# Kernel tuning notes

Measured on AMD Instinct MI355X. Metric: run time of the kernel, lower is better.

The kernel has to match this reference:

```python
import jax, jax.numpy as jnp
import numpy as np

E = 768      # embed_size
H = 12       # heads
L = 4        # num_length (stacked blocks)
N = 3072     # sequence length (and max_length)
FF = 4 * E   # feed-forward hidden
EPS = 1e-5


def layer_norm(x, g, b):
    mu = jnp.mean(x, axis=-1, keepdims=True)
    var = jnp.mean((x - mu) ** 2, axis=-1, keepdims=True)
    return (x - mu) / jnp.sqrt(var + EPS) * g + b


def setup_inputs() -> dict:
    key = jax.random.key(0)
    ks = jax.random.split(key, 12)
    inp = {
        "x": jax.random.normal(ks[0], (1, N, 768), dtype=jnp.float32),
        "mask": jnp.ones((1, N), dtype=jnp.int32),
        # 0.05 scale so word_encoding outputs have |.|>1 and survive the .long() truncation
        "W_word": jax.random.normal(ks[1], (E, 768), dtype=jnp.float32) * 0.05,
        "b_word": jnp.zeros((E,), dtype=jnp.float32),
        "pos_emb": jax.random.normal(ks[2], (N, E), dtype=jnp.float32),
        "Wq": jax.random.normal(ks[3], (L, E, E), dtype=jnp.float32) * 0.02,
        "Wk": jax.random.normal(ks[4], (L, E, E), dtype=jnp.float32) * 0.02,
        "Wv": jax.random.normal(ks[5], (L, E, E), dtype=jnp.float32) * 0.02,
        "Wo": jax.random.normal(ks[6], (L, E, E), dtype=jnp.float32) * 0.02,
        "W1": jax.random.normal(ks[7], (L, FF, E), dtype=jnp.float32) * 0.02,
        "b1": jnp.zeros((L, FF), dtype=jnp.float32),
        "W2": jax.random.normal(ks[8], (L, E, FF), dtype=jnp.float32) * 0.02,
        "b2": jnp.zeros((L, E), dtype=jnp.float32),
        "g1": jnp.ones((L, E), dtype=jnp.float32),
        "beta1": jnp.zeros((L, E), dtype=jnp.float32),
        "g2": jnp.ones((L, E), dtype=jnp.float32),
        "beta2": jnp.zeros((L, E), dtype=jnp.float32),
    }
    return inp


def reference(x, mask, W_word, b_word, pos_emb, Wq, Wk, Wv, Wo,
              W1, b1, W2, b2, g1, beta1, g2, beta2):
    # mask is squeezed then passed, but the original uses a non-inplace
    # masked_fill whose result is discarded -> mask has NO effect on the math.
    xs = x[0]                                # [N, 768]
    h = xs @ W_word.T + b_word               # word_encoding -> [N, E]
    h = jnp.trunc(h)                         # faithful to `x = x.long()` (cast truncation)
    n = h.shape[0]
    out = (h + pos_emb[:n])[None]            # [1, N, E]; dropout is identity (eval)
    d = E // H
    scale = jnp.asarray(E ** 0.5, out.dtype)  # softmax scaled by sqrt(embed_size)
    for l in range(L):
        q = (out @ Wq[l].T).reshape(1, n, H, d)
        k = (out @ Wk[l].T).reshape(1, n, H, d)
        v = (out @ Wv[l].T).reshape(1, n, H, d)
        energy = jnp.einsum('nqhd,nkhd->nhqk', q, k)      # [1, H, N, N]
        attn = jax.nn.softmax(energy / scale, axis=3)
        a = jnp.einsum('nhqk,nkhd->nqhd', attn, v).reshape(1, n, E) @ Wo[l].T
        xm = layer_norm(a + out, g1[l], beta1[l])
        y = jax.nn.relu(xm @ W1[l].T + b1[l]) @ W2[l].T + b2[l]
        out = layer_norm(xm + y, g2[l], beta2[l])
    return jnp.mean(out, axis=1, keepdims=True)          # [1, 1, E]
```

## Files before the change

kernel.cpp:

```cpp
#include <hip/hip_runtime.h>

#define E_  768
#define N_  3072
#define L_  4
#define H_  12
#define FF_ 3072
#define LDQKV 2304
#define SCL_ 0.052058744f

typedef short bf16x8 __attribute__((ext_vector_type(8)));
typedef short s16x4  __attribute__((ext_vector_type(4)));
typedef float f32x4  __attribute__((ext_vector_type(4)));
typedef __fp16 h16x2 __attribute__((ext_vector_type(2)));
typedef _Float16 f16x4 __attribute__((ext_vector_type(4)));
typedef _Float16 f16x8 __attribute__((ext_vector_type(8)));

__device__ __forceinline__ short f2bf(float f) {
  union { float f; unsigned u; } v; v.f = f;
  unsigned r = v.u + 0x7fffu + ((v.u >> 16) & 1u);
  return (short)(r >> 16);
}
__device__ __forceinline__ float bf2f(short s) {
  union { unsigned u; float f; } v; v.u = ((unsigned)(unsigned short)s) << 16;
  return v.f;
}

__device__ __forceinline__ void gld_lds16(const void* g, void* l) {
  __builtin_amdgcn_global_load_lds(
      (const __attribute__((address_space(1))) unsigned int*)g,
      (__attribute__((address_space(3))) unsigned int*)l, 16, 0, 0);
}

__global__ __launch_bounds__(256) void gemm_bt_kernel(
    const short* __restrict__ A, const short* __restrict__ B,
    const float* __restrict__ bias, float* __restrict__ Cf,
    short* __restrict__ Cb, _Float16* __restrict__ Vt,
    int Nd, int lda, int ldb, int kcnt, size_t czstride, int relu)
{
  alignas(16) __shared__ short As[128 * 32];
  alignas(16) __shared__ short Bs[128 * 32];
  const int tid = threadIdx.x;
  const int w = tid >> 6, lane = tid & 63;
  const int quad = lane >> 4, cl = lane & 15;
  const int wr = w >> 1, wc = w & 1;
  const int row0 = blockIdx.y * 128, col0 = blockIdx.x * 128;
  const int koff = blockIdx.z * kcnt;
  A += koff; B += koff;
  if (Cf) Cf += (size_t)blockIdx.z * czstride;
  const int srow = lane >> 2;
  const int scol = (((lane & 3) ^ ((lane >> 3) & 3)) * 8);
  const int rsw = (quad ^ ((cl >> 1) & 3)) * 8;
  const f32x4 fz = {0.f, 0.f, 0.f, 0.f};
  f32x4 acc[4][4];
#pragma unroll
  for (int i = 0; i < 4; i++)
#pragma unroll
    for (int j = 0; j < 4; j++) acc[i][j] = fz;

  const int nk = kcnt >> 5;
  for (int kt = 0; kt < nk; kt++) {
    const int k0 = kt << 5;
#pragma unroll
    for (int i = 0; i < 2; i++) {
      const int chunk = w * 2 + i;
      gld_lds16(A + (size_t)(row0 + chunk * 16 + srow) * lda + k0 + scol, As + chunk * 512);
      gld_lds16(B + (size_t)(col0 + chunk * 16 + srow) * ldb + k0 + scol, Bs + chunk * 512);
    }
    __syncthreads();
    bf16x8 af[4], bfr[4];
#pragma unroll
    for (int mt = 0; mt < 4; mt++)
      af[mt] = *(const bf16x8*)(As + (wr * 64 + mt * 16 + cl) * 32 + rsw);
#pragma unroll
    for (int nt = 0; nt < 4; nt++)
      bfr[nt] = *(const bf16x8*)(Bs + (wc * 64 + nt * 16 + cl) * 32 + rsw);
#pragma unroll
    for (int mt = 0; mt < 4; mt++)
#pragma unroll
      for (int nt = 0; nt < 4; nt++)
        acc[mt][nt] = __builtin_amdgcn_mfma_f32_16x16x32_bf16(af[mt], bfr[nt], acc[mt][nt], 0, 0, 0);
    __syncthreads();
  }
#pragma unroll
  for (int mt = 0; mt < 4; mt++)
#pragma unroll
    for (int nt = 0; nt < 4; nt++) {
      const int col = col0 + wc * 64 + nt * 16 + cl;
      const float bv = bias ? bias[col] : 0.f;
#pragma unroll
      for (int r = 0; r < 4; r++) {
        const int row = row0 + wr * 64 + mt * 16 + quad * 4 + r;
        float v2 = acc[mt][nt][r] + bv;
        if (relu) v2 = fmaxf(v2, 0.f);
        if (Cf) Cf[(size_t)row * Nd + col] = v2;
        if (Cb) Cb[(size_t)row * Nd + col] = f2bf(v2);
      }
      if (Vt && col >= 1536) {
        const int d = col - 1536;
        const int rowb = row0 + wr * 64 + mt * 16 + quad * 4;
        f16x4 vo;
#pragma unroll
        for (int r = 0; r < 4; r++) vo[r] = (_Float16)acc[mt][nt][r];
        *(f16x4*)(Vt + (size_t)d * N_ + rowb) = vo;
      }
    }
}

__global__ __launch_bounds__(256) void flash_kernel(
    const short* __restrict__ QKV, const _Float16* __restrict__ Vt,
    float* __restrict__ Op, float* __restrict__ Ml)
{
  alignas(16) __shared__ short Ks[64 * 64];
  alignas(16) __shared__ _Float16 Vs[64 * 64];
  const int tid = threadIdx.x;
  const int w = tid >> 6, lane = tid & 63;
  const int quad = lane >> 4, cl = lane & 15;
  const int q0 = blockIdx.x * 64, h = blockIdx.y, s = blockIdx.z;
  const int hoff = h * 64;
  const f32x4 fz = {0.f, 0.f, 0.f, 0.f};
  const int qrow = q0 + w * 16 + cl;
  const short* qp = QKV + (size_t)qrow * LDQKV + hoff;
  const bf16x8 bq0 = *(const bf16x8*)(qp + quad * 8);
  const bf16x8 bq1 = *(const bf16x8*)(qp + 32 + quad * 8);

  const int strow = lane >> 3;
  const int stcol = ((lane & 7) ^ strow) * 8;
  const short* kp0 = QKV + (size_t)(s * 768 + w * 16 + strow) * LDQKV + 768 + hoff + stcol;
  const short* kp1 = kp0 + 8 * LDQKV;
  const _Float16* vp0 = Vt + (size_t)(hoff + w * 16 + strow) * N_ + s * 768 + stcol;
  const _Float16* vp1 = vp0 + 8 * N_;
  short* ksd = Ks + w * 1024;
  _Float16* vsd = Vs + w * 1024;

  const int swz = cl & 7;
  const short* kf0 = Ks + cl * 64 + ((quad ^ swz) * 8);
  const short* kf1 = Ks + cl * 64 + (((quad + 4) ^ swz) * 8);
  const _Float16* vf0 = Vs + cl * 64 + (((0 + (quad >> 1)) ^ swz) * 8) + (quad & 1) * 4;
  const _Float16* vf1 = Vs + cl * 64 + (((2 + (quad >> 1)) ^ swz) * 8) + (quad & 1) * 4;
  const _Float16* vf2 = Vs + cl * 64 + (((4 + (quad >> 1)) ^ swz) * 8) + (quad & 1) * 4;
  const _Float16* vf3 = Vs + cl * 64 + (((6 + (quad >> 1)) ^ swz) * 8) + (quad & 1) * 4;

  f32x4 Oa[4];
#pragma unroll
  for (int t = 0; t < 4; t++) Oa[t] = fz;
  float l = 0.f;

  for (int kb = 0; kb < 12; kb++) {
    gld_lds16(kp0, ksd);
    gld_lds16(kp1, ksd + 512);
    gld_lds16(vp0, vsd);
    gld_lds16(vp1, vsd + 512);
    kp0 += 64 * LDQKV; kp1 += 64 * LDQKV; vp0 += 64; vp1 += 64;
    __syncthreads();
    f32x4 S[4];
#pragma unroll
    for (int t = 0; t < 4; t++) {
      const bf16x8 ak0 = *(const bf16x8*)(kf0 + t * 1024);
      const bf16x8 ak1 = *(const bf16x8*)(kf1 + t * 1024);
      f32x4 z = fz;
      z = __builtin_amdgcn_mfma_f32_16x16x32_bf16(ak0, bq0, z, 0, 0, 0);
      S[t] = __builtin_amdgcn_mfma_f32_16x16x32_bf16(ak1, bq1, z, 0, 0, 0);
    }
    f16x4 pf[4];
#pragma unroll
    for (int t = 0; t < 4; t++) {
      const float p0 = __builtin_amdgcn_exp2f(S[t][0]);
      const float p1 = __builtin_amdgcn_exp2f(S[t][1]);
      const float p2 = __builtin_amdgcn_exp2f(S[t][2]);
      const float p3 = __builtin_amdgcn_exp2f(S[t][3]);
      l += (p0 + p1) + (p2 + p3);
      const h16x2 lo = __builtin_amdgcn_cvt_pkrtz(p0, p1);
      const h16x2 hi = __builtin_amdgcn_cvt_pkrtz(p2, p3);
      pf[t][0] = (_Float16)lo[0]; pf[t][1] = (_Float16)lo[1];
      pf[t][2] = (_Float16)hi[0]; pf[t][3] = (_Float16)hi[1];
    }
#pragma unroll
    for (int td = 0; td < 4; td++) {
      Oa[td] = __builtin_amdgcn_mfma_f32_16x16x16f16(*(const f16x4*)(vf0 + td * 1024), pf[0], Oa[td], 0, 0, 0);
      Oa[td] = __builtin_amdgcn_mfma_f32_16x16x16f16(*(const f16x4*)(vf1 + td * 1024), pf[1], Oa[td], 0, 0, 0);
      Oa[td] = __builtin_amdgcn_mfma_f32_16x16x16f16(*(const f16x4*)(vf2 + td * 1024), pf[2], Oa[td], 0, 0, 0);
      Oa[td] = __builtin_amdgcn_mfma_f32_16x16x16f16(*(const f16x4*)(vf3 + td * 1024), pf[3], Oa[td], 0, 0, 0);
    }
    __syncthreads();
  }
  l += __shfl_xor(l, 16);
  l += __shfl_xor(l, 32);
  float* op = Op + ((size_t)s * N_ + qrow) * E_ + hoff;
#pragma unroll
  for (int td = 0; td < 4; td++)
#pragma unroll
    for (int r = 0; r < 4; r++)
      op[td * 16 + quad * 4 + r] = Oa[td][r];
  if (quad == 0)
    Ml[((size_t)s * H_ + h) * N_ + qrow] = l;
}

__global__ __launch_bounds__(256) void merge_kernel(
    const float* __restrict__ Op, const float* __restrict__ Ml,
    short* __restrict__ atb)
{
  const int idx = blockIdx.x * 256 + threadIdx.x;
  const int n = idx / 192, c4 = idx % 192;
  const int e0 = c4 * 4, h = e0 >> 6;
  float den = 0.f;
  f32x4 num = {0.f, 0.f, 0.f, 0.f};
#pragma unroll
  for (int s = 0; s < 4; s++) {
    den += Ml[((size_t)s * H_ + h) * N_ + n];
    const f32x4 o = *(const f32x4*)(Op + ((size_t)s * N_ + n) * E_ + e0);
#pragma unroll
    for (int j = 0; j < 4; j++) num[j] += o[j];
  }
  const float inv = 1.f / den;
  s16x4 ob;
#pragma unroll
  for (int j = 0; j < 4; j++) ob[j] = f2bf(num[j] * inv);
  *(s16x4*)(atb + (size_t)n * E_ + e0) = ob;
}

__global__ __launch_bounds__(256) void wordenc_fin_kernel(
    const float* __restrict__ p0, const float* __restrict__ p1,
    const float* __restrict__ bw, const float* __restrict__ pos,
    float* __restrict__ of, short* __restrict__ ob)
{
  const int idx = blockIdx.x * 256 + threadIdx.x;
  const size_t e4 = (size_t)idx * 4;
  const int cc = (int)(e4 % E_);
  const f32x4 a = *(const f32x4*)(p0 + e4);
  const f32x4 b = *(const f32x4*)(p1 + e4);
  const f32x4 bwv = *(const f32x4*)(bw + cc);
  const f32x4 pv = *(const f32x4*)(pos + e4);
  f32x4 o; s16x4 obv;
#pragma unroll
  for (int j = 0; j < 4; j++) {
    o[j] = truncf(a[j] + b[j] + bwv[j]) + pv[j];
    obv[j] = f2bf(o[j]);
  }
  *(f32x4*)(of + e4) = o;
  *(s16x4*)(ob + e4) = obv;
}

__global__ __launch_bounds__(256) void resid_ln_kernel(
    const float* __restrict__ a0, const float* __restrict__ a1,
    const float* __restrict__ a2, const float* __restrict__ a3,
    const float* __restrict__ b,
    const float* __restrict__ g, const float* __restrict__ bet,
    const float* __restrict__ bias,
    float* __restrict__ of, short* __restrict__ ob)
{
  const int row = blockIdx.x, tid = threadIdx.x;
  const int w = tid >> 6, lane = tid & 63;
  __shared__ float red[8];
  const size_t base = (size_t)row * E_;
  float v[3]; float s = 0.f;
#pragma unroll
  for (int j = 0; j < 3; j++) {
    const int cc = tid + j * 256;
    float t = (a0[base + cc] + a1[base + cc]) + (a2[base + cc] + a3[base + cc]) + b[base + cc];
    if (bias) t += bias[cc];
    v[j] = t;
    s += t;
  }
#pragma unroll
  for (int msk = 1; msk < 64; msk <<= 1) s += __shfl_xor(s, msk);
  if (lane == 0) red[w] = s;
  __syncthreads();
  const float mean = (red[0] + red[1] + red[2] + red[3]) * (1.f / E_);
  float s2 = 0.f;
#pragma unroll
  for (int j = 0; j < 3; j++) { const float d = v[j] - mean; s2 += d * d; }
#pragma unroll
  for (int msk = 1; msk < 64; msk <<= 1) s2 += __shfl_xor(s2, msk);
  if (lane == 0) red[4 + w] = s2;
  __syncthreads();
  const float var = (red[4] + red[5] + red[6] + red[7]) * (1.f / E_);
  const float rstd = rsqrtf(var + 1e-5f);
#pragma unroll
  for (int j = 0; j < 3; j++) {
    const int cc = tid + j * 256;
    const float o = (v[j] - mean) * rstd * g[cc] + bet[cc];
    of[base + cc] = o;
    ob[base + cc] = f2bf(o);
  }
}

__global__ __launch_bounds__(256) void prep_kernel(
    const float* __restrict__ Wq, const float* __restrict__ Wk,
    const float* __restrict__ Wv, const float* __restrict__ Wo,
    const float* __restrict__ W1, const float* __restrict__ W2,
    const float* __restrict__ Ww, const float* __restrict__ x,
    short* __restrict__ wqkv, short* __restrict__ wo_b,
    short* __restrict__ w1_b, short* __restrict__ w2_b,
    short* __restrict__ whl, short* __restrict__ xhl)
{
  int g = blockIdx.x * 256 + threadIdx.x;
  const int EEg = 589824;
  const int FEg = 2359296;
  if (g < 3 * EEg) {
    const int which = g / EEg;
    const int gi = g - which * EEg;
    const float* src = which == 0 ? Wq : (which == 1 ? Wk : Wv);
    const float scale = which == 0 ? SCL_ : 1.f;
    const size_t e4 = (size_t)gi * 4;
    const int lidx = (int)(e4 / (E_ * E_));
    const size_t rem = e4 % (E_ * E_);
    const f32x4 v = *(const f32x4*)(src + e4);
    s16x4 o;
#pragma unroll
    for (int q = 0; q < 4; q++) o[q] = f2bf(v[q] * scale);
    *(s16x4*)(wqkv + ((size_t)lidx * 3 + which) * E_ * E_ + rem) = o;
    return;
  }
  g -= 3 * EEg;
  if (g < EEg) {
    const size_t e4 = (size_t)g * 4;
    const f32x4 v = *(const f32x4*)(Wo + e4);
    s16x4 o;
#pragma unroll
    for (int q = 0; q < 4; q++) o[q] = f2bf(v[q]);
    *(s16x4*)(wo_b + e4) = o;
    return;
  }
  g -= EEg;
  if (g < FEg) {
    const size_t e4 = (size_t)g * 4;
    const f32x4 v = *(const f32x4*)(W1 + e4);
    s16x4 o;
#pragma unroll
    for (int q = 0; q < 4; q++) o[q] = f2bf(v[q]);
    *(s16x4*)(w1_b + e4) = o;
    return;
  }
  g -= FEg;
  if (g < FEg) {
    const size_t e4 = (size_t)g * 4;
    const f32x4 v = *(const f32x4*)(W2 + e4);
    s16x4 o;
#pragma unroll
    for (int q = 0; q < 4; q++) o[q] = f2bf(v[q]);
    *(s16x4*)(w2_b + e4) = o;
    return;
  }
  g -= FEg;
  if (g < 147456) {
    const size_t e4 = (size_t)g * 4;
    const int c = (int)(e4 / E_);
    const int k = (int)(e4 % E_);
    const f32x4 v = *(const f32x4*)(Ww + e4);
    s16x4 hi, lo;
#pragma unroll
    for (int q = 0; q < 4; q++) {
      hi[q] = f2bf(v[q]);
      lo[q] = f2bf(v[q] - bf2f(hi[q]));
    }
    short* base = whl + (size_t)c * LDQKV + k;
    *(s16x4*)(base) = hi;
    *(s16x4*)(base + 768) = hi;
    *(s16x4*)(base + 1536) = lo;
    return;
  }
  g -= 147456;
  {
    const size_t e4 = (size_t)g * 4;
    const int n = (int)(e4 / E_);
    const int k = (int)(e4 % E_);
    const f32x4 v = *(const f32x4*)(x + e4);
    s16x4 hi, lo;
#pragma unroll
    for (int q = 0; q < 4; q++) {
      hi[q] = f2bf(v[q]);
      lo[q] = f2bf(v[q] - bf2f(hi[q]));
    }
    short* base = xhl + (size_t)n * LDQKV + k;
    *(s16x4*)(base) = hi;
    *(s16x4*)(base + 768) = lo;
    *(s16x4*)(base + 1536) = hi;
  }
}

__global__ void colmean_kernel(const float* __restrict__ src, float* __restrict__ out)
{
  const int c = blockIdx.x * 256 + threadIdx.x;
  const int r0 = blockIdx.y * 128;
  float s = 0.f;
  for (int r = 0; r < 128; r++) s += src[(size_t)(r0 + r) * E_ + c];
  atomicAdd(&out[c], s * (1.f / N_));
}

extern "C" void kernel_launch(void* const* d_in, const int* in_sizes, int n_in,
                              void* d_out, int out_size, void* d_ws, size_t ws_size,
                              hipStream_t stream)
{
  (void)in_sizes; (void)n_in; (void)out_size; (void)ws_size;
  const float* x     = (const float*)d_in[0];
  const float* Wword = (const float*)d_in[2];
  const float* bword = (const float*)d_in[3];
  const float* pos   = (const float*)d_in[4];
  const float* Wq    = (const float*)d_in[5];
  const float* Wk    = (const float*)d_in[6];
  const float* Wv    = (const float*)d_in[7];
  const float* Wo    = (const float*)d_in[8];
  const float* W1    = (const float*)d_in[9];
  const float* b1    = (const float*)d_in[10];
  const float* W2    = (const float*)d_in[11];
  const float* b2    = (const float*)d_in[12];
  const float* g1    = (const float*)d_in[13];
  const float* be1   = (const float*)d_in[14];
  const float* g2    = (const float*)d_in[15];
  const float* be2   = (const float*)d_in[16];

  char* p = (char*)d_ws;
  auto take = [&](size_t bytes) { char* q = p; p += (bytes + 255) & ~(size_t)255; return q; };
  const size_t EE = (size_t)E_ * E_;
  const size_t NE = (size_t)N_ * E_;
  const size_t FE = (size_t)FF_ * E_;

  short* wqkv_b = (short*)take(L_ * 3 * EE * 2);
  short* wo_b   = (short*)take(L_ * EE * 2);
  short* w1_b   = (short*)take(L_ * FE * 2);
  short* w2_b   = (short*)take(L_ * FE * 2);
  short* whl    = (short*)take((size_t)E_ * LDQKV * 2);
  float* outf   = (float*)take(NE * 4);
  short* outb   = (short*)take(NE * 2);
  float* xmf    = (float*)take(NE * 4);
  short* xmb    = (short*)take(NE * 2);
  short* qkvb   = (short*)take((size_t)N_ * LDQKV * 2);
  float* Op     = (float*)take(4 * NE * 4);
  float* part4  = (float*)take(4 * NE * 4);
  float* Ml     = (float*)take((size_t)4 * H_ * N_ * 4);

  short* xhl  = qkvb;
  short* y1b  = (short*)Op;
  _Float16* vtb = (_Float16*)xmf;
  short* atb  = outb;

  prep_kernel<<<dim3(30528), dim3(256), 0, stream>>>(
      Wq, Wk, Wv, Wo, W1, W2, Wword, x,
      wqkv_b, wo_b, w1_b, w2_b, whl, xhl);

  gemm_bt_kernel<<<dim3(6, 24, 2), dim3(256), 0, stream>>>(
      xhl, whl, nullptr, Op, nullptr, nullptr, E_, LDQKV, LDQKV, 1152, NE, 0);
  wordenc_fin_kernel<<<dim3(2304), dim3(256), 0, stream>>>(
      Op, Op + NE, bword, pos, outf, outb);

  for (int l = 0; l < L_; l++) {
    gemm_bt_kernel<<<dim3(18, 24, 1), dim3(256), 0, stream>>>(
        outb, wqkv_b + l * 3 * EE, nullptr, nullptr, qkvb, vtb, LDQKV, E_, E_, E_, 0, 0);
    flash_kernel<<<dim3(48, 12, 4), dim3(256), 0, stream>>>(qkvb, vtb, Op, Ml);
    merge_kernel<<<dim3(2304), dim3(256), 0, stream>>>(Op, Ml, atb);
    gemm_bt_kernel<<<dim3(6, 24, 4), dim3(256), 0, stream>>>(
        atb, wo_b + l * EE, nullptr, Op, nullptr, nullptr, E_, E_, E_, 192, NE, 0);
    resid_ln_kernel<<<dim3(N_), dim3(256), 0, stream>>>(
        Op, Op + NE, Op + 2 * NE, Op + 3 * NE, outf,
        g1 + l * E_, be1 + l * E_, nullptr, xmf, xmb);
    gemm_bt_kernel<<<dim3(24, 24, 1), dim3(256), 0, stream>>>(
        xmb, w1_b + l * FE, b1 + l * FF_, nullptr, y1b, nullptr, FF_, E_, E_, E_, 0, 1);
    gemm_bt_kernel<<<dim3(6, 24, 4), dim3(256), 0, stream>>>(
        y1b, w2_b + l * FE, nullptr, part4, nullptr, nullptr, E_, FF_, FF_, 768, NE, 0);
    resid_ln_kernel<<<dim3(N_), dim3(256), 0, stream>>>(
        part4, part4 + NE, part4 + 2 * NE, part4 + 3 * NE, xmf,
        g2 + l * E_, be2 + l * E_, b2 + l * E_, outf, outb);
  }
  hipMemsetAsync(d_out, 0, E_ * sizeof(float), stream);
  colmean_kernel<<<dim3(3, 24), dim3(256), 0, stream>>>(outf, (float*)d_out);
}
```

Baseline: 994.8 us.

## Restructure flash attention: per-wave key split, double-buffered LDS, in-block reduction

The flash kernel now gives each wave all 64 query rows of the block and its own slice of the keys, instead of a 16-row slice sharing keys with the other waves. Each wave streams its keys through a private double-buffered LDS area using async global-to-LDS loads and vmcnt waits, so the per-iteration block barriers go away. The four waves' partial outputs are then reduced through LDS at the end. This halves the key split across blocks, so the merge kernel reads two partials instead of four. It costs more accumulator registers (16 f32x4 per wave) and a final LDS reduction, which may lower occupancy. Separately, the prep kernel processes two elements per thread with half as many blocks.

```diff
diff --git a/kernel.cpp b/kernel.cpp
--- a/kernel.cpp
+++ b/kernel.cpp
@@ -13,7 +13,6 @@
 typedef float f32x4  __attribute__((ext_vector_type(4)));
 typedef __fp16 h16x2 __attribute__((ext_vector_type(2)));
 typedef _Float16 f16x4 __attribute__((ext_vector_type(4)));
-typedef _Float16 f16x8 __attribute__((ext_vector_type(8)));
 
 __device__ __forceinline__ short f2bf(float f) {
   union { float f; unsigned u; } v; v.f = f;
@@ -110,89 +109,157 @@
     const short* __restrict__ QKV, const _Float16* __restrict__ Vt,
     float* __restrict__ Op, float* __restrict__ Ml)
 {
-  alignas(16) __shared__ short Ks[64 * 64];
-  alignas(16) __shared__ _Float16 Vs[64 * 64];
+  alignas(16) __shared__ short KV[16640];
   const int tid = threadIdx.x;
   const int w = tid >> 6, lane = tid & 63;
   const int quad = lane >> 4, cl = lane & 15;
   const int q0 = blockIdx.x * 64, h = blockIdx.y, s = blockIdx.z;
   const int hoff = h * 64;
   const f32x4 fz = {0.f, 0.f, 0.f, 0.f};
-  const int qrow = q0 + w * 16 + cl;
-  const short* qp = QKV + (size_t)qrow * LDQKV + hoff;
-  const bf16x8 bq0 = *(const bf16x8*)(qp + quad * 8);
-  const bf16x8 bq1 = *(const bf16x8*)(qp + 32 + quad * 8);
-
-  const int strow = lane >> 3;
-  const int stcol = ((lane & 7) ^ strow) * 8;
-  const short* kp0 = QKV + (size_t)(s * 768 + w * 16 + strow) * LDQKV + 768 + hoff + stcol;
+
+  bf16x8 bq[4][2];
+#pragma unroll
+  for (int qt = 0; qt < 4; qt++)
+#pragma unroll
+    for (int c = 0; c < 2; c++)
+      bq[qt][c] = *(const bf16x8*)(QKV + (size_t)(q0 + qt * 16 + cl) * LDQKV + hoff + c * 32 + quad * 8);
+
+  const int kr0 = s * 1536 + w * 384;
+  const short* kp0 = QKV + (size_t)(kr0 + (lane >> 3)) * LDQKV + 768 + hoff + ((lane & 7) ^ (lane >> 3)) * 8;
   const short* kp1 = kp0 + 8 * LDQKV;
-  const _Float16* vp0 = Vt + (size_t)(hoff + w * 16 + strow) * N_ + s * 768 + stcol;
-  const _Float16* vp1 = vp0 + 8 * N_;
-  short* ksd = Ks + w * 1024;
-  _Float16* vsd = Vs + w * 1024;
-
-  const int swz = cl & 7;
-  const short* kf0 = Ks + cl * 64 + ((quad ^ swz) * 8);
-  const short* kf1 = Ks + cl * 64 + (((quad + 4) ^ swz) * 8);
-  const _Float16* vf0 = Vs + cl * 64 + (((0 + (quad >> 1)) ^ swz) * 8) + (quad & 1) * 4;
-  const _Float16* vf1 = Vs + cl * 64 + (((2 + (quad >> 1)) ^ swz) * 8) + (quad & 1) * 4;
-  const _Float16* vf2 = Vs + cl * 64 + (((4 + (quad >> 1)) ^ swz) * 8) + (quad & 1) * 4;
-  const _Float16* vf3 = Vs + cl * 64 + (((6 + (quad >> 1)) ^ swz) * 8) + (quad & 1) * 4;
-
-  f32x4 Oa[4];
-#pragma unroll
-  for (int t = 0; t < 4; t++) Oa[t] = fz;
-  float l = 0.f;
-
-  for (int kb = 0; kb < 12; kb++) {
-    gld_lds16(kp0, ksd);
-    gld_lds16(kp1, ksd + 512);
-    gld_lds16(vp0, vsd);
-    gld_lds16(vp1, vsd + 512);
-    kp0 += 64 * LDQKV; kp1 += 64 * LDQKV; vp0 += 64; vp1 += 64;
-    __syncthreads();
+  const _Float16* vp0 = Vt + (size_t)(hoff + (lane >> 1)) * N_ + kr0 + (lane & 1) * 8;
+  const _Float16* vp1 = vp0 + 32 * N_;
+  short* kb0 = KV + w * 4096;
+  short* kb1 = KV + w * 4096 + 1024;
+  short* vb0 = KV + w * 4096 + 2048;
+  short* vb1 = KV + w * 4096 + 3072;
+
+  f32x4 Oa[16];
+#pragma unroll
+  for (int t = 0; t < 16; t++) Oa[t] = fz;
+  float l4[4] = {0.f, 0.f, 0.f, 0.f};
+
+  gld_lds16(kp0, kb0); gld_lds16(kp1, kb0 + 512);
+  gld_lds16(vp0, vb0); gld_lds16(vp1, vb0 + 512);
+  kp0 += 16 * LDQKV; kp1 += 16 * LDQKV; vp0 += 16; vp1 += 16;
+
+  for (int it = 0; it < 24; it++) {
+    const int cur = it & 1;
+    {
+      short* kn = cur ? kb0 : kb1;
+      short* vn = cur ? vb0 : vb1;
+      gld_lds16(kp0, kn); gld_lds16(kp1, kn + 512);
+      gld_lds16(vp0, vn); gld_lds16(vp1, vn + 512);
+      kp0 += 16 * LDQKV; kp1 += 16 * LDQKV; vp0 += 16; vp1 += 16;
+    }
+    asm volatile("s_waitcnt vmcnt(4)" ::: "memory");
+    const short* kc = (cur ? kb1 : kb0) + cl * 64;
+    const _Float16* vc = (const _Float16*)(cur ? vb1 : vb0);
+    const bf16x8 ak0 = *(const bf16x8*)(kc + ((quad ^ (cl & 7)) * 8));
+    const bf16x8 ak1 = *(const bf16x8*)(kc + (((quad + 4) ^ (cl & 7)) * 8));
     f32x4 S[4];
 #pragma unroll
-    for (int t = 0; t < 4; t++) {
-      const bf16x8 ak0 = *(const bf16x8*)(kf0 + t * 1024);
-      const bf16x8 ak1 = *(const bf16x8*)(kf1 + t * 1024);
+    for (int qt = 0; qt < 4; qt++) {
       f32x4 z = fz;
-      z = __builtin_amdgcn_mfma_f32_16x16x32_bf16(ak0, bq0, z, 0, 0, 0);
-      S[t] = __builtin_amdgcn_mfma_f32_16x16x32_bf16(ak1, bq1, z, 0, 0, 0);
+      z = __builtin_amdgcn_mfma_f32_16x16x32_bf16(ak0, bq[qt][0], z, 0, 0, 0);
+      S[qt] = __builtin_amdgcn_mfma_f32_16x16x32_bf16(ak1, bq[qt][1], z, 0, 0, 0);
     }
     f16x4 pf[4];
 #pragma unroll
-    for (int t = 0; t < 4; t++) {
-      const float p0 = __builtin_amdgcn_exp2f(S[t][0]);
-      const float p1 = __builtin_amdgcn_exp2f(S[t][1]);
-      const float p2 = __builtin_amdgcn_exp2f(S[t][2]);
-      const float p3 = __builtin_amdgcn_exp2f(S[t][3]);
-      l += (p0 + p1) + (p2 + p3);
+    for (int qt = 0; qt < 4; qt++) {
+      const float p0 = __builtin_amdgcn_exp2f(S[qt][0]);
+      const float p1 = __builtin_amdgcn_exp2f(S[qt][1]);
+      const float p2 = __builtin_amdgcn_exp2f(S[qt][2]);
+      const float p3 = __builtin_amdgcn_exp2f(S[qt][3]);
+      l4[qt] += (p0 + p1) + (p2 + p3);
       const h16x2 lo = __builtin_amdgcn_cvt_pkrtz(p0, p1);
       const h16x2 hi = __builtin_amdgcn_cvt_pkrtz(p2, p3);
-      pf[t][0] = (_Float16)lo[0]; pf[t][1] = (_Float16)lo[1];
-      pf[t][2] = (_Float16)hi[0]; pf[t][3] = (_Float16)hi[1];
-    }
-#pragma unroll
-    for (int td = 0; td < 4; td++) {
-      Oa[td] = __builtin_amdgcn_mfma_f32_16x16x16f16(*(const f16x4*)(vf0 + td * 1024), pf[0], Oa[td], 0, 0, 0);
-      Oa[td] = __builtin_amdgcn_mfma_f32_16x16x16f16(*(const f16x4*)(vf1 + td * 1024), pf[1], Oa[td], 0, 0, 0);
-      Oa[td] = __builtin_amdgcn_mfma_f32_16x16x16f16(*(const f16x4*)(vf2 + td * 1024), pf[2], Oa[td], 0, 0, 0);
-      Oa[td] = __builtin_amdgcn_mfma_f32_16x16x16f16(*(const f16x4*)(vf3 + td * 1024), pf[3], Oa[td], 0, 0, 0);
-    }
-    __syncthreads();
-  }
-  l += __shfl_xor(l, 16);
-  l += __shfl_xor(l, 32);
-  float* op = Op + ((size_t)s * N_ + qrow) * E_ + hoff;
-#pragma unroll
-  for (int td = 0; td < 4; td++)
-#pragma unroll
-    for (int r = 0; r < 4; r++)
-      op[td * 16 + quad * 4 + r] = Oa[td][r];
-  if (quad == 0)
-    Ml[((size_t)s * H_ + h) * N_ + qrow] = l;
+      pf[qt][0] = (_Float16)lo[0]; pf[qt][1] = (_Float16)lo[1];
+      pf[qt][2] = (_Float16)hi[0]; pf[qt][3] = (_Float16)hi[1];
+    }
+#pragma unroll
+    for (int dt = 0; dt < 4; dt++) {
+      const f16x4 av = *(const f16x4*)(vc + dt * 256 + cl * 16 + quad * 4);
+#pragma unroll
+      for (int qt = 0; qt < 4; qt++)
+        Oa[dt * 4 + qt] = __builtin_amdgcn_mfma_f32_16x16x16f16(av, pf[qt], Oa[dt * 4 + qt], 0, 0, 0);
+    }
+  }
+#pragma unroll
+  for (int qt = 0; qt < 4; qt++) {
+    l4[qt] += __shfl_xor(l4[qt], 16);
+    l4[qt] += __shfl_xor(l4[qt], 32);
+  }
+
+  asm volatile("s_waitcnt vmcnt(0)" ::: "memory");
+
+  float* comb = (float*)KV;
+  float* lA = (float*)(KV + 16384);
+  float* lB = lA + 64;
+  __syncthreads();
+  if (w & 1) {
+    float* dst = comb + (w == 1 ? 0 : 4096);
+#pragma unroll
+    for (int t = 0; t < 16; t++) *(f32x4*)(dst + t * 256 + lane * 4) = Oa[t];
+    float* ld = (w == 1) ? lA : lB;
+    if (quad == 0)
+#pragma unroll
+      for (int qt = 0; qt < 4; qt++) ld[qt * 16 + cl] = l4[qt];
+  }
+  __syncthreads();
+  if (w == 0) {
+#pragma unroll
+    for (int t = 0; t < 16; t++) {
+      const f32x4 o = *(const f32x4*)(comb + t * 256 + lane * 4);
+#pragma unroll
+      for (int r = 0; r < 4; r++) Oa[t][r] += o[r];
+    }
+#pragma unroll
+    for (int qt = 0; qt < 4; qt++) l4[qt] += lA[qt * 16 + cl];
+  }
+  if (w == 2) {
+#pragma unroll
+    for (int t = 0; t < 16; t++) {
+      const f32x4 o = *(const f32x4*)(comb + 4096 + t * 256 + lane * 4);
+#pragma unroll
+      for (int r = 0; r < 4; r++) Oa[t][r] += o[r];
+    }
+#pragma unroll
+    for (int qt = 0; qt < 4; qt++) l4[qt] += lB[qt * 16 + cl];
+  }
+  __syncthreads();
+  if (w == 2) {
+#pragma unroll
+    for (int t = 0; t < 16; t++) *(f32x4*)(comb + t * 256 + lane * 4) = Oa[t];
+    if (quad == 0)
+#pragma unroll
+      for (int qt = 0; qt < 4; qt++) lA[qt * 16 + cl] = l4[qt];
+  }
+  __syncthreads();
+  if (w == 0) {
+#pragma unroll
+    for (int t = 0; t < 16; t++) {
+      const f32x4 o = *(const f32x4*)(comb + t * 256 + lane * 4);
+#pragma unroll
+      for (int r = 0; r < 4; r++) Oa[t][r] += o[r];
+    }
+#pragma unroll
+    for (int qt = 0; qt < 4; qt++) l4[qt] += lA[qt * 16 + cl];
+    float* opb = Op + (size_t)s * (N_ * E_);
+#pragma unroll
+    for (int qt = 0; qt < 4; qt++) {
+      float* oprow = opb + (size_t)(q0 + qt * 16 + cl) * E_ + hoff;
+#pragma unroll
+      for (int dt = 0; dt < 4; dt++)
+#pragma unroll
+        for (int r = 0; r < 4; r++)
+          oprow[dt * 16 + quad * 4 + r] = Oa[dt * 4 + qt][r];
+    }
+    if (quad == 0)
+#pragma unroll
+      for (int qt = 0; qt < 4; qt++)
+        Ml[((size_t)s * H_ + h) * N_ + q0 + qt * 16 + cl] = l4[qt];
+  }
 }
 
 __global__ __launch_bounds__(256) void merge_kernel(
@@ -205,7 +272,7 @@
   float den = 0.f;
   f32x4 num = {0.f, 0.f, 0.f, 0.f};
 #pragma unroll
-  for (int s = 0; s < 4; s++) {
+  for (int s = 0; s < 2; s++) {
     den += Ml[((size_t)s * H_ + h) * N_ + n];
     const f32x4 o = *(const f32x4*)(Op + ((size_t)s * N_ + n) * E_ + e0);
 #pragma unroll
@@ -293,88 +360,92 @@
     short* __restrict__ w1_b, short* __restrict__ w2_b,
     short* __restrict__ whl, short* __restrict__ xhl)
 {
-  int g = blockIdx.x * 256 + threadIdx.x;
+  const int idx = blockIdx.x * 256 + threadIdx.x;
   const int EEg = 589824;
   const int FEg = 2359296;
-  if (g < 3 * EEg) {
-    const int which = g / EEg;
-    const int gi = g - which * EEg;
-    const float* src = which == 0 ? Wq : (which == 1 ? Wk : Wv);
-    const float scale = which == 0 ? SCL_ : 1.f;
-    const size_t e4 = (size_t)gi * 4;
-    const int lidx = (int)(e4 / (E_ * E_));
-    const size_t rem = e4 % (E_ * E_);
-    const f32x4 v = *(const f32x4*)(src + e4);
-    s16x4 o;
-#pragma unroll
-    for (int q = 0; q < 4; q++) o[q] = f2bf(v[q] * scale);
-    *(s16x4*)(wqkv + ((size_t)lidx * 3 + which) * E_ * E_ + rem) = o;
-    return;
-  }
-  g -= 3 * EEg;
-  if (g < EEg) {
-    const size_t e4 = (size_t)g * 4;
-    const f32x4 v = *(const f32x4*)(Wo + e4);
-    s16x4 o;
-#pragma unroll
-    for (int q = 0; q < 4; q++) o[q] = f2bf(v[q]);
-    *(s16x4*)(wo_b + e4) = o;
-    return;
-  }
-  g -= EEg;
-  if (g < FEg) {
-    const size_t e4 = (size_t)g * 4;
-    const f32x4 v = *(const f32x4*)(W1 + e4);
-    s16x4 o;
-#pragma unroll
-    for (int q = 0; q < 4; q++) o[q] = f2bf(v[q]);
-    *(s16x4*)(w1_b + e4) = o;
-    return;
-  }
-  g -= FEg;
-  if (g < FEg) {
-    const size_t e4 = (size_t)g * 4;
-    const f32x4 v = *(const f32x4*)(W2 + e4);
-    s16x4 o;
-#pragma unroll
-    for (int q = 0; q < 4; q++) o[q] = f2bf(v[q]);
-    *(s16x4*)(w2_b + e4) = o;
-    return;
-  }
-  g -= FEg;
-  if (g < 147456) {
-    const size_t e4 = (size_t)g * 4;
-    const int c = (int)(e4 / E_);
-    const int k = (int)(e4 % E_);
-    const f32x4 v = *(const f32x4*)(Ww + e4);
-    s16x4 hi, lo;
-#pragma unroll
-    for (int q = 0; q < 4; q++) {
-      hi[q] = f2bf(v[q]);
-      lo[q] = f2bf(v[q] - bf2f(hi[q]));
-    }
-    short* base = whl + (size_t)c * LDQKV + k;
-    *(s16x4*)(base) = hi;
-    *(s16x4*)(base + 768) = hi;
-    *(s16x4*)(base + 1536) = lo;
-    return;
-  }
-  g -= 147456;
-  {
-    const size_t e4 = (size_t)g * 4;
-    const int n = (int)(e4 / E_);
-    const int k = (int)(e4 % E_);
-    const f32x4 v = *(const f32x4*)(x + e4);
-    s16x4 hi, lo;
-#pragma unroll
-    for (int q = 0; q < 4; q++) {
-      hi[q] = f2bf(v[q]);
-      lo[q] = f2bf(v[q] - bf2f(hi[q]));
-    }
-    short* base = xhl + (size_t)n * LDQKV + k;
-    *(s16x4*)(base) = hi;
-    *(s16x4*)(base + 768) = lo;
-    *(s16x4*)(base + 1536) = hi;
+#pragma unroll
+  for (int u = 0; u < 2; u++) {
+    int g = idx * 2 + u;
+    if (g < 3 * EEg) {
+      const int which = g / EEg;
+      const int gi = g - which * EEg;
+      const float* src = which == 0 ? Wq : (which == 1 ? Wk : Wv);
+      const float scale = which == 0 ? SCL_ : 1.f;
+      const size_t e4 = (size_t)gi * 4;
+      const int lidx = (int)(e4 / (E_ * E_));
+      const size_t rem = e4 % (E_ * E_);
+      const f32x4 v = *(const f32x4*)(src + e4);
+      s16x4 o;
+#pragma unroll
+      for (int q = 0; q < 4; q++) o[q] = f2bf(v[q] * scale);
+      *(s16x4*)(wqkv + ((size_t)lidx * 3 + which) * E_ * E_ + rem) = o;
+      continue;
+    }
+    g -= 3 * EEg;
+    if (g < EEg) {
+      const size_t e4 = (size_t)g * 4;
+      const f32x4 v = *(const f32x4*)(Wo + e4);
+      s16x4 o;
+#pragma unroll
+      for (int q = 0; q < 4; q++) o[q] = f2bf(v[q]);
+      *(s16x4*)(wo_b + e4) = o;
+      continue;
+    }
+    g -= EEg;
+    if (g < FEg) {
+      const size_t e4 = (size_t)g * 4;
+      const f32x4 v = *(const f32x4*)(W1 + e4);
+      s16x4 o;
+#pragma unroll
+      for (int q = 0; q < 4; q++) o[q] = f2bf(v[q]);
+      *(s16x4*)(w1_b + e4) = o;
+      continue;
+    }
+    g -= FEg;
+    if (g < FEg) {
+      const size_t e4 = (size_t)g * 4;
+      const f32x4 v = *(const f32x4*)(W2 + e4);
+      s16x4 o;
+#pragma unroll
+      for (int q = 0; q < 4; q++) o[q] = f2bf(v[q]);
+      *(s16x4*)(w2_b + e4) = o;
+      continue;
+    }
+    g -= FEg;
+    if (g < 147456) {
+      const size_t e4 = (size_t)g * 4;
+      const int c = (int)(e4 / E_);
+      const int k = (int)(e4 % E_);
+      const f32x4 v = *(const f32x4*)(Ww + e4);
+      s16x4 hi, lo;
+#pragma unroll
+      for (int q = 0; q < 4; q++) {
+        hi[q] = f2bf(v[q]);
+        lo[q] = f2bf(v[q] - bf2f(hi[q]));
+      }
+      short* base = whl + (size_t)c * LDQKV + k;
+      *(s16x4*)(base) = hi;
+      *(s16x4*)(base + 768) = hi;
+      *(s16x4*)(base + 1536) = lo;
+      continue;
+    }
+    g -= 147456;
+    {
+      const size_t e4 = (size_t)g * 4;
+      const int n = (int)(e4 / E_);
+      const int k = (int)(e4 % E_);
+      const f32x4 v = *(const f32x4*)(x + e4);
+      s16x4 hi, lo;
+#pragma unroll
+      for (int q = 0; q < 4; q++) {
+        hi[q] = f2bf(v[q]);
+        lo[q] = f2bf(v[q] - bf2f(hi[q]));
+      }
+      short* base = xhl + (size_t)n * LDQKV + k;
+      *(s16x4*)(base) = hi;
+      *(s16x4*)(base + 768) = lo;
+      *(s16x4*)(base + 1536) = hi;
+    }
   }
 }
 
@@ -427,14 +498,14 @@
   short* qkvb   = (short*)take((size_t)N_ * LDQKV * 2);
   float* Op     = (float*)take(4 * NE * 4);
   float* part4  = (float*)take(4 * NE * 4);
-  float* Ml     = (float*)take((size_t)4 * H_ * N_ * 4);
+  float* Ml     = (float*)take((size_t)2 * H_ * N_ * 4);
 
   short* xhl  = qkvb;
   short* y1b  = (short*)Op;
   _Float16* vtb = (_Float16*)xmf;
   short* atb  = outb;
 
-  prep_kernel<<<dim3(30528), dim3(256), 0, stream>>>(
+  prep_kernel<<<dim3(15264), dim3(256), 0, stream>>>(
       Wq, Wk, Wv, Wo, W1, W2, Wword, x,
       wqkv_b, wo_b, w1_b, w2_b, whl, xhl);
 
@@ -446,7 +517,7 @@
   for (int l = 0; l < L_; l++) {
     gemm_bt_kernel<<<dim3(18, 24, 1), dim3(256), 0, stream>>>(
         outb, wqkv_b + l * 3 * EE, nullptr, nullptr, qkvb, vtb, LDQKV, E_, E_, E_, 0, 0);
-    flash_kernel<<<dim3(48, 12, 4), dim3(256), 0, stream>>>(qkvb, vtb, Op, Ml);
+    flash_kernel<<<dim3(48, 12, 2), dim3(256), 0, stream>>>(qkvb, vtb, Op, Ml);
     merge_kernel<<<dim3(2304), dim3(256), 0, stream>>>(Op, Ml, atb);
     gemm_bt_kernel<<<dim3(6, 24, 4), dim3(256), 0, stream>>>(
         atb, wo_b + l * EE, nullptr, Op, nullptr, nullptr, E_, E_, E_, 192, NE, 0);
```

Result: slower. 1.066 ms (+7.1%).

## Add 128x64-tile GEMM for QKV and FFN1, process two elements per prep thread

Applied to the files above, without the earlier changes.

Adds a smaller-tile GEMM kernel (128x64 output tile, 4 waves each owning 32 rows, single-buffered global-to-LDS loads) and uses it for the QKV projection and the first FFN GEMM in place of the larger-tile kernel. The grids grow from 432 and 576 blocks to 864 and 1152, which should fill the GPU's compute units better and cut tail waves. Separately, each prep_kernel thread now converts two 4-element chunks, halving the launched blocks. The smaller tiles give less data reuse per LDS load and add more global traffic.

```diff
diff --git a/kernel.cpp b/kernel.cpp
--- a/kernel.cpp
+++ b/kernel.cpp
@@ -13,7 +13,6 @@
 typedef float f32x4  __attribute__((ext_vector_type(4)));
 typedef __fp16 h16x2 __attribute__((ext_vector_type(2)));
 typedef _Float16 f16x4 __attribute__((ext_vector_type(4)));
-typedef _Float16 f16x8 __attribute__((ext_vector_type(8)));
 
 __device__ __forceinline__ short f2bf(float f) {
   union { float f; unsigned u; } v; v.f = f;
@@ -106,6 +105,75 @@
     }
 }
 
+__global__ __launch_bounds__(256) void gemm64_kernel(
+    const short* __restrict__ A, const short* __restrict__ B,
+    const float* __restrict__ bias, short* __restrict__ Cb,
+    _Float16* __restrict__ Vt, int Nd, int lda, int ldb, int kcnt, int relu)
+{
+  alignas(16) __shared__ short As[128 * 32];
+  alignas(16) __shared__ short Bs[64 * 32];
+  const int tid = threadIdx.x;
+  const int w = tid >> 6, lane = tid & 63;
+  const int quad = lane >> 4, cl = lane & 15;
+  const int row0 = blockIdx.y * 128, col0 = blockIdx.x * 64;
+  const int srow = lane >> 2;
+  const int scol = (((lane & 3) ^ ((lane >> 3) & 3)) * 8);
+  const int rsw = (quad ^ ((cl >> 1) & 3)) * 8;
+  const f32x4 fz = {0.f, 0.f, 0.f, 0.f};
+  f32x4 acc[2][4];
+#pragma unroll
+  for (int i = 0; i < 2; i++)
+#pragma unroll
+    for (int j = 0; j < 4; j++) acc[i][j] = fz;
+
+  const int nk = kcnt >> 5;
+  for (int kt = 0; kt < nk; kt++) {
+    const int k0 = kt << 5;
+#pragma unroll
+    for (int i = 0; i < 2; i++) {
+      const int chunk = w * 2 + i;
+      gld_lds16(A + (size_t)(row0 + chunk * 16 + srow) * lda + k0 + scol, As + chunk * 512);
+    }
+    gld_lds16(B + (size_t)(col0 + w * 16 + srow) * ldb + k0 + scol, Bs + w * 512);
+    __syncthreads();
+    bf16x8 af[2], bfr[4];
+#pragma unroll
+    for (int mt = 0; mt < 2; mt++)
+      af[mt] = *(const bf16x8*)(As + (w * 32 + mt * 16 + cl) * 32 + rsw);
+#pragma unroll
+    for (int nt = 0; nt < 4; nt++)
+      bfr[nt] = *(const bf16x8*)(Bs + (nt * 16 + cl) * 32 + rsw);
+#pragma unroll
+    for (int mt = 0; mt < 2; mt++)
+#pragma unroll
+      for (int nt = 0; nt < 4; nt++)
+        acc[mt][nt] = __builtin_amdgcn_mfma_f32_16x16x32_bf16(af[mt], bfr[nt], acc[mt][nt], 0, 0, 0);
+    __syncthreads();
+  }
+#pragma unroll
+  for (int mt = 0; mt < 2; mt++)
+#pragma unroll
+    for (int nt = 0; nt < 4; nt++) {
+      const int col = col0 + nt * 16 + cl;
+      const float bv = bias ? bias[col] : 0.f;
+#pragma unroll
+      for (int r = 0; r < 4; r++) {
+        const int row = row0 + w * 32 + mt * 16 + quad * 4 + r;
+        float v2 = acc[mt][nt][r] + bv;
+        if (relu) v2 = fmaxf(v2, 0.f);
+        Cb[(size_t)row * Nd + col] = f2bf(v2);
+      }
+      if (Vt && col >= 1536) {
+        const int d = col - 1536;
+        const int rowb = row0 + w * 32 + mt * 16 + quad * 4;
+        f16x4 vo;
+#pragma unroll
+        for (int r = 0; r < 4; r++) vo[r] = (_Float16)acc[mt][nt][r];
+        *(f16x4*)(Vt + (size_t)d * N_ + rowb) = vo;
+      }
+    }
+}
+
 __global__ __launch_bounds__(256) void flash_kernel(
     const short* __restrict__ QKV, const _Float16* __restrict__ Vt,
     float* __restrict__ Op, float* __restrict__ Ml)
@@ -293,88 +361,92 @@
     short* __restrict__ w1_b, short* __restrict__ w2_b,
     short* __restrict__ whl, short* __restrict__ xhl)
 {
-  int g = blockIdx.x * 256 + threadIdx.x;
+  const int idx = blockIdx.x * 256 + threadIdx.x;
   const int EEg = 589824;
   const int FEg = 2359296;
-  if (g < 3 * EEg) {
-    const int which = g / EEg;
-    const int gi = g - which * EEg;
-    const float* src = which == 0 ? Wq : (which == 1 ? Wk : Wv);
-    const float scale = which == 0 ? SCL_ : 1.f;
-    const size_t e4 = (size_t)gi * 4;
-    const int lidx = (int)(e4 / (E_ * E_));
-    const size_t rem = e4 % (E_ * E_);
-    const f32x4 v = *(const f32x4*)(src + e4);
-    s16x4 o;
-#pragma unroll
-    for (int q = 0; q < 4; q++) o[q] = f2bf(v[q] * scale);
-    *(s16x4*)(wqkv + ((size_t)lidx * 3 + which) * E_ * E_ + rem) = o;
-    return;
-  }
-  g -= 3 * EEg;
-  if (g < EEg) {
-    const size_t e4 = (size_t)g * 4;
-    const f32x4 v = *(const f32x4*)(Wo + e4);
-    s16x4 o;
-#pragma unroll
-    for (int q = 0; q < 4; q++) o[q] = f2bf(v[q]);
-    *(s16x4*)(wo_b + e4) = o;
-    return;
-  }
-  g -= EEg;
-  if (g < FEg) {
-    const size_t e4 = (size_t)g * 4;
-    const f32x4 v = *(const f32x4*)(W1 + e4);
-    s16x4 o;
-#pragma unroll
-    for (int q = 0; q < 4; q++) o[q] = f2bf(v[q]);
-    *(s16x4*)(w1_b + e4) = o;
-    return;
-  }
-  g -= FEg;
-  if (g < FEg) {
-    const size_t e4 = (size_t)g * 4;
-    const f32x4 v = *(const f32x4*)(W2 + e4);
-    s16x4 o;
-#pragma unroll
-    for (int q = 0; q < 4; q++) o[q] = f2bf(v[q]);
-    *(s16x4*)(w2_b + e4) = o;
-    return;
-  }
-  g -= FEg;
-  if (g < 147456) {
-    const size_t e4 = (size_t)g * 4;
-    const int c = (int)(e4 / E_);
-    const int k = (int)(e4 % E_);
-    const f32x4 v = *(const f32x4*)(Ww + e4);
-    s16x4 hi, lo;
-#pragma unroll
-    for (int q = 0; q < 4; q++) {
-      hi[q] = f2bf(v[q]);
-      lo[q] = f2bf(v[q] - bf2f(hi[q]));
-    }
-    short* base = whl + (size_t)c * LDQKV + k;
-    *(s16x4*)(base) = hi;
-    *(s16x4*)(base + 768) = hi;
-    *(s16x4*)(base + 1536) = lo;
-    return;
-  }
-  g -= 147456;
-  {
-    const size_t e4 = (size_t)g * 4;
-    const int n = (int)(e4 / E_);
-    const int k = (int)(e4 % E_);
-    const f32x4 v = *(const f32x4*)(x + e4);
-    s16x4 hi, lo;
-#pragma unroll
-    for (int q = 0; q < 4; q++) {
-      hi[q] = f2bf(v[q]);
-      lo[q] = f2bf(v[q] - bf2f(hi[q]));
-    }
-    short* base = xhl + (size_t)n * LDQKV + k;
-    *(s16x4*)(base) = hi;
-    *(s16x4*)(base + 768) = lo;
-    *(s16x4*)(base + 1536) = hi;
+#pragma unroll
+  for (int u = 0; u < 2; u++) {
+    int g = idx * 2 + u;
+    if (g < 3 * EEg) {
+      const int which = g / EEg;
+      const int gi = g - which * EEg;
+      const float* src = which == 0 ? Wq : (which == 1 ? Wk : Wv);
+      const float scale = which == 0 ? SCL_ : 1.f;
+      const size_t e4 = (size_t)gi * 4;
+      const int lidx = (int)(e4 / (E_ * E_));
+      const size_t rem = e4 % (E_ * E_);
+      const f32x4 v = *(const f32x4*)(src + e4);
+      s16x4 o;
+#pragma unroll
+      for (int q = 0; q < 4; q++) o[q] = f2bf(v[q] * scale);
+      *(s16x4*)(wqkv + ((size_t)lidx * 3 + which) * E_ * E_ + rem) = o;
+      continue;
+    }
+    g -= 3 * EEg;
+    if (g < EEg) {
+      const size_t e4 = (size_t)g * 4;
+      const f32x4 v = *(const f32x4*)(Wo + e4);
+      s16x4 o;
+#pragma unroll
+      for (int q = 0; q < 4; q++) o[q] = f2bf(v[q]);
+      *(s16x4*)(wo_b + e4) = o;
+      continue;
+    }
+    g -= EEg;
+    if (g < FEg) {
+      const size_t e4 = (size_t)g * 4;
+      const f32x4 v = *(const f32x4*)(W1 + e4);
+      s16x4 o;
+#pragma unroll
+      for (int q = 0; q < 4; q++) o[q] = f2bf(v[q]);
+      *(s16x4*)(w1_b + e4) = o;
+      continue;
+    }
+    g -= FEg;
+    if (g < FEg) {
+      const size_t e4 = (size_t)g * 4;
+      const f32x4 v = *(const f32x4*)(W2 + e4);
+      s16x4 o;
+#pragma unroll
+      for (int q = 0; q < 4; q++) o[q] = f2bf(v[q]);
+      *(s16x4*)(w2_b + e4) = o;
+      continue;
+    }
+    g -= FEg;
+    if (g < 147456) {
+      const size_t e4 = (size_t)g * 4;
+      const int c = (int)(e4 / E_);
+      const int k = (int)(e4 % E_);
+      const f32x4 v = *(const f32x4*)(Ww + e4);
+      s16x4 hi, lo;
+#pragma unroll
+      for (int q = 0; q < 4; q++) {
+        hi[q] = f2bf(v[q]);
+        lo[q] = f2bf(v[q] - bf2f(hi[q]));
+      }
+      short* base = whl + (size_t)c * LDQKV + k;
+      *(s16x4*)(base) = hi;
+      *(s16x4*)(base + 768) = hi;
+      *(s16x4*)(base + 1536) = lo;
+      continue;
+    }
+    g -= 147456;
+    {
+      const size_t e4 = (size_t)g * 4;
+      const int n = (int)(e4 / E_);
+      const int k = (int)(e4 % E_);
+      const f32x4 v = *(const f32x4*)(x + e4);
+      s16x4 hi, lo;
+#pragma unroll
+      for (int q = 0; q < 4; q++) {
+        hi[q] = f2bf(v[q]);
+        lo[q] = f2bf(v[q] - bf2f(hi[q]));
+      }
+      short* base = xhl + (size_t)n * LDQKV + k;
+      *(s16x4*)(base) = hi;
+      *(s16x4*)(base + 768) = lo;
+      *(s16x4*)(base + 1536) = hi;
+    }
   }
 }
 
@@ -434,7 +506,7 @@
   _Float16* vtb = (_Float16*)xmf;
   short* atb  = outb;
 
-  prep_kernel<<<dim3(30528), dim3(256), 0, stream>>>(
+  prep_kernel<<<dim3(15264), dim3(256), 0, stream>>>(
       Wq, Wk, Wv, Wo, W1, W2, Wword, x,
       wqkv_b, wo_b, w1_b, w2_b, whl, xhl);
 
@@ -444,8 +516,8 @@
       Op, Op + NE, bword, pos, outf, outb);
 
   for (int l = 0; l < L_; l++) {
-    gemm_bt_kernel<<<dim3(18, 24, 1), dim3(256), 0, stream>>>(
-        outb, wqkv_b + l * 3 * EE, nullptr, nullptr, qkvb, vtb, LDQKV, E_, E_, E_, 0, 0);
+    gemm64_kernel<<<dim3(36, 24), dim3(256), 0, stream>>>(
+        outb, wqkv_b + l * 3 * EE, nullptr, qkvb, vtb, LDQKV, E_, E_, E_, 0);
     flash_kernel<<<dim3(48, 12, 4), dim3(256), 0, stream>>>(qkvb, vtb, Op, Ml);
     merge_kernel<<<dim3(2304), dim3(256), 0, stream>>>(Op, Ml, atb);
     gemm_bt_kernel<<<dim3(6, 24, 4), dim3(256), 0, stream>>>(
@@ -453,8 +525,8 @@
     resid_ln_kernel<<<dim3(N_), dim3(256), 0, stream>>>(
         Op, Op + NE, Op + 2 * NE, Op + 3 * NE, outf,
         g1 + l * E_, be1 + l * E_, nullptr, xmf, xmb);
-    gemm_bt_kernel<<<dim3(24, 24, 1), dim3(256), 0, stream>>>(
-        xmb, w1_b + l * FE, b1 + l * FF_, nullptr, y1b, nullptr, FF_, E_, E_, E_, 0, 1);
+    gemm64_kernel<<<dim3(48, 24), dim3(256), 0, stream>>>(
+        xmb, w1_b + l * FE, b1 + l * FF_, y1b, nullptr, FF_, E_, E_, E_, 1);
     gemm_bt_kernel<<<dim3(6, 24, 4), dim3(256), 0, stream>>>(
         y1b, w2_b + l * FE, nullptr, part4, nullptr, nullptr, E_, FF_, FF_, 768, NE, 0);
     resid_ln_kernel<<<dim3(N_), dim3(256), 0, stream>>>(
```

New measurement: 997.6 us. No clear change (+0.3%).
